# Kernel optimization log

Measured on AMD Instinct MI355X. Metric: run time of the kernel, lower is better.

The kernel has to match this reference:

```python
import jax, jax.numpy as jnp
from jax import lax
import numpy as np

EPS = 1e-5
RADIUS = 0.2
NPOINT = 1024
NSAMPLE = 32
B, N = 8, 8192


def furthest_point_sample(xyz, npoint):
    # xyz: (B,N,3) -> idx (B,npoint), start at index 0 (pytorch3d default)
    Bn, Nn, _ = xyz.shape
    def step(carry, _):
        dists, last = carry  # (B,N), (B,)
        lastpt = jnp.take_along_axis(xyz, last[:, None, None], axis=1)  # (B,1,3)
        d = jnp.sum((xyz - lastpt) ** 2, axis=-1)  # (B,N)
        dists = jnp.minimum(dists, d)
        nxt = jnp.argmax(dists, axis=-1).astype(jnp.int32)
        return (dists, nxt), last
    init = (jnp.full((Bn, Nn), jnp.inf, xyz.dtype), jnp.zeros((Bn,), jnp.int32))
    _, idxs = lax.scan(step, init, None, length=npoint)  # (npoint,B)
    return idxs.T  # (B,npoint)


def ball_query(radius, nsample, xyz, new_xyz):
    # first `nsample` points (by original index order) within radius; pad -> 0 (clamp of -1)
    Nn = xyz.shape[1]
    d2 = jnp.sum((new_xyz[:, :, None, :] - xyz[:, None, :, :]) ** 2, axis=-1)  # (B,S,N)
    valid = d2 < radius * radius
    score = jnp.where(valid, jnp.arange(Nn, dtype=jnp.int32), jnp.int32(Nn))  # smaller = earlier valid
    neg_vals, _ = lax.top_k(-score, nsample)  # picks nsample smallest scores
    idx = -neg_vals  # (B,S,nsample)
    idx = jnp.where(idx == Nn, 0, idx)  # pytorch3d pads with -1, then clamp(min=0) -> 0
    return idx


def bn_relu(x, g, be, m, v):
    # eval-mode BatchNorm over channel (last) dim + ReLU
    return jax.nn.relu((x - m) * (g / jnp.sqrt(v + EPS)) + be)


def setup_inputs() -> dict:
    key = jax.random.key(0)
    ks = jax.random.split(key, 4)
    xyz = jax.random.uniform(ks[0], (B, N, 3), dtype=jnp.float32)
    w1 = jax.random.normal(ks[1], (64, 3), dtype=jnp.float32) * 0.1
    w2 = jax.random.normal(ks[2], (64, 64), dtype=jnp.float32) * 0.1
    w3 = jax.random.normal(ks[3], (128, 64), dtype=jnp.float32) * 0.1
    z64, o64 = jnp.zeros((64,), jnp.float32), jnp.ones((64,), jnp.float32)
    z128, o128 = jnp.zeros((128,), jnp.float32), jnp.ones((128,), jnp.float32)
    return {
        "xyz": xyz,
        "w1": w1, "b1": z64, "g1": o64, "be1": z64, "m1": z64, "v1": o64,
        "w2": w2, "b2": z64, "g2": o64, "be2": z64, "m2": z64, "v2": o64,
        "w3": w3, "b3": z128, "g3": o128, "be3": z128, "m3": z128, "v3": o128,
    }


def reference(xyz, w1, b1, g1, be1, m1, v1, w2, b2, g2, be2, m2, v2, w3, b3, g3, be3, m3, v3):
    fps_idx = furthest_point_sample(xyz, NPOINT)  # (B,npoint)
    new_xyz = jnp.take_along_axis(xyz, fps_idx[:, :, None], axis=1)  # (B,npoint,3)
    idx = ball_query(RADIUS, NSAMPLE, xyz, new_xyz)  # (B,npoint,nsample)
    grouped_xyz = jax.vmap(lambda pts, i: pts[i])(xyz, idx)  # (B,npoint,nsample,3)
    # 1x1 conv MLP (channels-last) + eval BN + ReLU
    h = bn_relu(jnp.einsum('bsnc,oc->bsno', grouped_xyz, w1) + b1, g1, be1, m1, v1)
    h = bn_relu(jnp.einsum('bsnc,oc->bsno', h, w2) + b2, g2, be2, m2, v2)
    h = bn_relu(jnp.einsum('bsnc,oc->bsno', h, w3) + b3, g3, be3, m3, v3)
    new_features = jnp.max(h, axis=2)  # (B,npoint,128) max over nsample
    new_features = jnp.transpose(new_features, (0, 2, 1))  # (B,128,npoint) to match torch layout
    return new_xyz, new_features
```

## Files before the change

### kernel.cpp

```cpp
#include <hip/hip_runtime.h>

#define B 8
#define N 8192
#define S 1024
#define NS 32
#define THREADS 512
#define NCONS_BLK 248
#define NCONS_WAVE (NCONS_BLK * 8)
constexpr float BN_EPS = 1e-5f;

typedef float v2f __attribute__((ext_vector_type(2)));

struct KParams {
  const float* xyz;
  const float *w1, *b1, *g1, *be1, *m1, *v1;
  const float *w2, *b2, *g2, *be2, *m2, *v2;
  const float *w3, *b3, *g3, *be3, *m3, *v3;
  float* new_xyz;
  float* out_feat;
  float* ctrs;
  unsigned* prog;
};

__device__ __forceinline__ float wave_max_to_lane63(float x) {
  int v = __float_as_int(x);
#define DPP_MAX(ctrl)                                                     \
  v = __float_as_int(fmaxf(__int_as_float(v),                             \
      __int_as_float(__builtin_amdgcn_update_dpp(v, v, (ctrl), 0xf, 0xf, \
                                                 false))))
  DPP_MAX(0x111);
  DPP_MAX(0x112);
  DPP_MAX(0x114);
  DPP_MAX(0x118);
  DPP_MAX(0x142);
  DPP_MAX(0x143);
#undef DPP_MAX
  return __int_as_float(v);
}

__device__ __forceinline__ void producer(const KParams& P, char* smem, int b,
                                         int t, int lane, int w) {
#pragma clang fp contract(off)
  float4* s_xyz4 = (float4*)smem;
  float* s_ctr = (float*)(smem + 131072);
  unsigned long long(*s_red)[8] =
      (unsigned long long(*)[8])(smem + 131072 + 12288);
  const float* base = P.xyz + (size_t)b * N * 3;
  v2f X[8], Y[8], Z[8], D[8];
  const int p0 = t * 16;
  {
    const float4* src = (const float4*)(base + (size_t)p0 * 3);
    float buf[48];
#pragma unroll
    for (int i = 0; i < 12; ++i) {
      float4 v = src[i];
      buf[4 * i + 0] = v.x; buf[4 * i + 1] = v.y;
      buf[4 * i + 2] = v.z; buf[4 * i + 3] = v.w;
    }
#pragma unroll
    for (int k = 0; k < 16; ++k)
      s_xyz4[p0 + k] =
          make_float4(buf[3 * k], buf[3 * k + 1], buf[3 * k + 2], 0.f);
#pragma unroll
    for (int i = 0; i < 8; ++i) {
      X[i] = (v2f){buf[6 * i + 0], buf[6 * i + 3]};
      Y[i] = (v2f){buf[6 * i + 1], buf[6 * i + 4]};
      Z[i] = (v2f){buf[6 * i + 2], buf[6 * i + 5]};
      D[i] = (v2f){3.4e38f, 3.4e38f};
    }
  }
  float lx = base[0], ly = base[1], lz = base[2];
  if (t == 0) { s_ctr[0] = lx; s_ctr[1] = ly; s_ctr[2] = lz; }
  for (int r = 1; r < S; ++r) {
    v2f lx2 = lx, ly2 = ly, lz2 = lz;
#pragma unroll
    for (int i = 0; i < 8; ++i) {
      v2f dx = X[i] - lx2, dy = Y[i] - ly2, dz = Z[i] - lz2;
      v2f d = (dx * dx + dy * dy) + dz * dz;
      D[i] = __builtin_elementwise_min(D[i], d);
    }
    float n1[8], n2[4], n3[2];
#pragma unroll
    for (int i = 0; i < 8; ++i) n1[i] = fmaxf(D[i].x, D[i].y);
#pragma unroll
    for (int i = 0; i < 4; ++i) n2[i] = fmaxf(n1[2 * i], n1[2 * i + 1]);
    n3[0] = fmaxf(n2[0], n2[1]);
    n3[1] = fmaxf(n2[2], n2[3]);
    float m = fmaxf(n3[0], n3[1]);
    int c3 = (n3[0] < m) ? 1 : 0;
    float n2s = c3 ? n2[2] : n2[0];
    int c2 = (n2s < m) ? 1 : 0;
    float n1a = c3 ? n1[4] : n1[0];
    float n1b = c3 ? n1[6] : n1[2];
    float n1s = c2 ? n1b : n1a;
    int c1 = (n1s < m) ? 1 : 0;
    float dx0 = c3 ? D[4].x : D[0].x;
    float dx1 = c3 ? D[5].x : D[1].x;
    float dx2 = c3 ? D[6].x : D[2].x;
    float dx3 = c3 ? D[7].x : D[3].x;
    float dxa = c2 ? dx2 : dx0;
    float dxb = c2 ? dx3 : dx1;
    float dxs = c1 ? dxb : dxa;
    int c0 = (dxs < m) ? 1 : 0;
    int li = 8 * c3 + 4 * c2 + 2 * c1 + c0;
    float wm = wave_max_to_lane63(m);
    float wavemax =
        __int_as_float(__builtin_amdgcn_readlane(__float_as_int(wm), 63));
    unsigned long long bal = __ballot(m == wavemax);
    int firstlane = (int)__builtin_ctzll(bal);
    int widx = __builtin_amdgcn_readlane(p0 + li, firstlane);
    unsigned long long key =
        ((unsigned long long)__float_as_uint(wavemax) << 32) |
        (unsigned)(8191 - widx);
    if (lane == 0) s_red[r & 1][w] = key;
    __syncthreads();
    {
      const unsigned long long* sr = s_red[r & 1];
      unsigned long long k0 = sr[0], k1 = sr[1], k2 = sr[2], k3 = sr[3];
      unsigned long long k4 = sr[4], k5 = sr[5], k6 = sr[6], k7 = sr[7];
      unsigned long long a = k0 > k1 ? k0 : k1;
      unsigned long long c = k2 > k3 ? k2 : k3;
      unsigned long long e = k4 > k5 ? k4 : k5;
      unsigned long long g = k6 > k7 ? k6 : k7;
      unsigned long long ac = a > c ? a : c;
      unsigned long long eg = e > g ? e : g;
      unsigned long long kmax = ac > eg ? ac : eg;
      const int bi = 8191 - (int)(unsigned)(kmax & 0xffffffffull);
      float4 cc = s_xyz4[bi];
      lx = cc.x; ly = cc.y; lz = cc.z;
    }
    if (t == 0) {
      s_ctr[r * 3 + 0] = lx; s_ctr[r * 3 + 1] = ly; s_ctr[r * 3 + 2] = lz;
    }
    if (w == 0 && (r & 7) == 7) {
      int cbase = (r - 7) * 3;
      if (lane < 24) {
        float v = s_ctr[cbase + lane];
        __hip_atomic_store(P.ctrs + (size_t)b * (S * 3) + cbase + lane, v,
                           __ATOMIC_RELAXED, __HIP_MEMORY_SCOPE_AGENT);
      }
      if (lane == 0)
        __hip_atomic_store(&P.prog[b * 64], (unsigned)(r + 1),
                           __ATOMIC_RELEASE, __HIP_MEMORY_SCOPE_AGENT);
    }
  }
  __syncthreads();
  float* o = P.new_xyz + (size_t)b * S * 3;
  for (int i = t; i < (S * 3) / 4; i += THREADS)
    ((float4*)o)[i] = ((const float4*)s_ctr)[i];
}

__device__ __forceinline__ void consumer(const KParams& P, char* smem, int cid,
                                         int t, int lane, int w) {
#pragma clang fp contract(off)
  constexpr float R2 = (float)(0.2 * 0.2);
  float* h = (float*)smem + w * (NS * 64);
  float* cs = (float*)smem + 8 * NS * 64 + w * (NS * 4);
  const unsigned gw = cid * 8 + w;
  float sv1 = P.g1[lane] / sqrtf(P.v1[lane] + BN_EPS);
  float bb1 = (P.b1[lane] - P.m1[lane]) * sv1 + P.be1[lane];
  float w1x = P.w1[lane * 3 + 0] * sv1, w1y = P.w1[lane * 3 + 1] * sv1,
        w1z = P.w1[lane * 3 + 2] * sv1;
  float sv2 = P.g2[lane] / sqrtf(P.v2[lane] + BN_EPS);
  float bb2 = (P.b2[lane] - P.m2[lane]) * sv2 + P.be2[lane];
  float W2[64];
#pragma unroll
  for (int k = 0; k < 64; k += 4) {
    float4 q = *(const float4*)(P.w2 + lane * 64 + k);
    W2[k + 0] = q.x * sv2; W2[k + 1] = q.y * sv2;
    W2[k + 2] = q.z * sv2; W2[k + 3] = q.w * sv2;
  }
  float sva = P.g3[lane] / sqrtf(P.v3[lane] + BN_EPS);
  float bba = (P.b3[lane] - P.m3[lane]) * sva + P.be3[lane];
  float svb = P.g3[lane + 64] / sqrtf(P.v3[lane + 64] + BN_EPS);
  float bbb = (P.b3[lane + 64] - P.m3[lane + 64]) * svb + P.be3[lane + 64];
  float Wa[64], Wb[64];
#pragma unroll
  for (int k = 0; k < 64; k += 4) {
    float4 qa = *(const float4*)(P.w3 + lane * 64 + k);
    Wa[k + 0] = qa.x * sva; Wa[k + 1] = qa.y * sva;
    Wa[k + 2] = qa.z * sva; Wa[k + 3] = qa.w * sva;
    float4 qb = *(const float4*)(P.w3 + (lane + 64) * 64 + k);
    Wb[k + 0] = qb.x * svb; Wb[k + 1] = qb.y * svb;
    Wb[k + 2] = qb.z * svb; Wb[k + 3] = qb.w * svb;
  }
  for (unsigned c = gw; c < B * S; c += NCONS_WAVE) {
    const int b = c & 7;
    const int s = c >> 3;
    while (__hip_atomic_load(&P.prog[b * 64], __ATOMIC_RELAXED,
                             __HIP_MEMORY_SCOPE_AGENT) <= (unsigned)s)
      __builtin_amdgcn_s_sleep(2);
    (void)__hip_atomic_load(&P.prog[b * 64], __ATOMIC_ACQUIRE,
                            __HIP_MEMORY_SCOPE_AGENT);
    const float* cg = P.ctrs + (size_t)b * (S * 3) + s * 3;
    float cx = __hip_atomic_load(cg + 0, __ATOMIC_RELAXED,
                                 __HIP_MEMORY_SCOPE_AGENT);
    float cy = __hip_atomic_load(cg + 1, __ATOMIC_RELAXED,
                                 __HIP_MEMORY_SCOPE_AGENT);
    float cz = __hip_atomic_load(cg + 2, __ATOMIC_RELAXED,
                                 __HIP_MEMORY_SCOPE_AGENT);
    const float* base = P.xyz + (size_t)b * N * 3;
    int cnt = 0;
    for (int c0 = 0; c0 < N && cnt < NS; c0 += 64) {
      int p = c0 + lane;
      float x = base[p * 3], y = base[p * 3 + 1], z = base[p * 3 + 2];
      float dx = x - cx, dy = y - cy, dz = z - cz;
      float d = (dx * dx + dy * dy) + dz * dz;
      bool v = d < R2;
      unsigned long long mk = __ballot(v);
      int rank = cnt + __popcll(mk & ((1ull << lane) - 1ull));
      if (v && rank < NS) {
        cs[rank * 4 + 0] = x; cs[rank * 4 + 1] = y; cs[rank * 4 + 2] = z;
      }
      cnt += (int)__popcll(mk);
    }
    if (cnt < NS) {
      float x0 = base[0], y0 = base[1], z0 = base[2];
      for (int j = cnt + lane; j < NS; j += 64) {
        cs[j * 4 + 0] = x0; cs[j * 4 + 1] = y0; cs[j * 4 + 2] = z0;
      }
    }
    for (int n = 0; n < NS; ++n) {
      float a = fmaf(w1x, cs[n * 4 + 0],
                     fmaf(w1y, cs[n * 4 + 1], fmaf(w1z, cs[n * 4 + 2], bb1)));
      h[n * 64 + lane] = fmaxf(a, 0.f);
    }
    for (int n = 0; n < NS; ++n) {
      float acc = bb2;
#pragma unroll
      for (int k = 0; k < 64; k += 4) {
        float4 q = *(const float4*)(h + n * 64 + k);
        acc = fmaf(W2[k + 0], q.x, acc);
        acc = fmaf(W2[k + 1], q.y, acc);
        acc = fmaf(W2[k + 2], q.z, acc);
        acc = fmaf(W2[k + 3], q.w, acc);
      }
      h[n * 64 + lane] = fmaxf(acc, 0.f);
    }
    float mxa = 0.f, mxb = 0.f;
    for (int n = 0; n < NS; ++n) {
      float acca = bba, accb = bbb;
#pragma unroll
      for (int k = 0; k < 64; k += 4) {
        float4 q = *(const float4*)(h + n * 64 + k);
        acca = fmaf(Wa[k + 0], q.x, acca);
        acca = fmaf(Wa[k + 1], q.y, acca);
        acca = fmaf(Wa[k + 2], q.z, acca);
        acca = fmaf(Wa[k + 3], q.w, acca);
        accb = fmaf(Wb[k + 0], q.x, accb);
        accb = fmaf(Wb[k + 1], q.y, accb);
        accb = fmaf(Wb[k + 2], q.z, accb);
        accb = fmaf(Wb[k + 3], q.w, accb);
      }
      mxa = fmaxf(mxa, acca);
      mxb = fmaxf(mxb, accb);
    }
    P.out_feat[((size_t)b * 128 + lane) * S + s] = mxa;
    P.out_feat[((size_t)b * 128 + 64 + lane) * S + s] = mxb;
  }
}

__global__ void __attribute__((amdgpu_flat_work_group_size(THREADS, THREADS),
                               amdgpu_waves_per_eu(2, 2)))
k_fused(KParams P) {
  extern __shared__ char smem[];
  const int t = threadIdx.x;
  const int lane = t & 63;
  const int w = t >> 6;
  if (blockIdx.x < B)
    producer(P, smem, blockIdx.x, t, lane, w);
  else
    consumer(P, smem, blockIdx.x - B, t, lane, w);
}

extern "C" void kernel_launch(void* const* d_in, const int* in_sizes, int n_in,
                              void* d_out, int out_size, void* d_ws,
                              size_t ws_size, hipStream_t stream) {
  KParams P;
  P.xyz = (const float*)d_in[0];
  P.w1 = (const float*)d_in[1];  P.b1 = (const float*)d_in[2];
  P.g1 = (const float*)d_in[3];  P.be1 = (const float*)d_in[4];
  P.m1 = (const float*)d_in[5];  P.v1 = (const float*)d_in[6];
  P.w2 = (const float*)d_in[7];  P.b2 = (const float*)d_in[8];
  P.g2 = (const float*)d_in[9];  P.be2 = (const float*)d_in[10];
  P.m2 = (const float*)d_in[11]; P.v2 = (const float*)d_in[12];
  P.w3 = (const float*)d_in[13]; P.b3 = (const float*)d_in[14];
  P.g3 = (const float*)d_in[15]; P.be3 = (const float*)d_in[16];
  P.m3 = (const float*)d_in[17]; P.v3 = (const float*)d_in[18];
  float* out = (float*)d_out;
  P.new_xyz = out;
  P.out_feat = out + (size_t)B * S * 3;
  P.prog = (unsigned*)d_ws;
  P.ctrs = (float*)((char*)d_ws + 2048);

  hipMemsetAsync(d_ws, 0, 2048, stream);

  void* args[] = {&P};
  dim3 grid(B + NCONS_BLK), blk(THREADS);
  size_t shmem = 131072 + 12288 + 256;
  hipError_t e = hipLaunchCooperativeKernel((const void*)k_fused, grid, blk,
                                            args, (unsigned)shmem, stream);
  if (e != hipSuccess) {
    k_fused<<<grid, blk, shmem, stream>>>(P);
  }
}
```

Measured before the change: 1.049 ms.

## Halve block size so FPS threads own more points, with lagged progress publish

Block size drops from 512 to 256 threads. Each FPS producer thread now holds 32 points in registers, and the cross-wave argmax reduces over 4 waves instead of 8. This is meant to shorten the per-iteration barrier and reduction on the serial FPS critical path, at the cost of more per-thread arithmetic and register pressure, and half as many consumer waves per block. The progress counter is now published one batch late, ahead of the newest center stores, with a final publish after the loop. Consumer spin-wait sleep is also lengthened to reduce polling traffic.

```diff
diff --git a/kernel.cpp b/kernel.cpp
--- a/kernel.cpp
+++ b/kernel.cpp
@@ -4,9 +4,9 @@
 #define N 8192
 #define S 1024
 #define NS 32
-#define THREADS 512
+#define THREADS 256
 #define NCONS_BLK 248
-#define NCONS_WAVE (NCONS_BLK * 8)
+#define NCONS_WAVE (NCONS_BLK * 4)
 constexpr float BN_EPS = 1e-5f;
 
 typedef float v2f __attribute__((ext_vector_type(2)));
@@ -43,26 +43,26 @@
 #pragma clang fp contract(off)
   float4* s_xyz4 = (float4*)smem;
   float* s_ctr = (float*)(smem + 131072);
-  unsigned long long(*s_red)[8] =
-      (unsigned long long(*)[8])(smem + 131072 + 12288);
+  unsigned long long(*s_red)[4] =
+      (unsigned long long(*)[4])(smem + 131072 + 12288);
   const float* base = P.xyz + (size_t)b * N * 3;
-  v2f X[8], Y[8], Z[8], D[8];
-  const int p0 = t * 16;
+  v2f X[16], Y[16], Z[16], D[16];
+  const int p0 = t * 32;
   {
     const float4* src = (const float4*)(base + (size_t)p0 * 3);
-    float buf[48];
-#pragma unroll
-    for (int i = 0; i < 12; ++i) {
+    float buf[96];
+#pragma unroll
+    for (int i = 0; i < 24; ++i) {
       float4 v = src[i];
       buf[4 * i + 0] = v.x; buf[4 * i + 1] = v.y;
       buf[4 * i + 2] = v.z; buf[4 * i + 3] = v.w;
     }
 #pragma unroll
-    for (int k = 0; k < 16; ++k)
+    for (int k = 0; k < 32; ++k)
       s_xyz4[p0 + k] =
           make_float4(buf[3 * k], buf[3 * k + 1], buf[3 * k + 2], 0.f);
 #pragma unroll
-    for (int i = 0; i < 8; ++i) {
+    for (int i = 0; i < 16; ++i) {
       X[i] = (v2f){buf[6 * i + 0], buf[6 * i + 3]};
       Y[i] = (v2f){buf[6 * i + 1], buf[6 * i + 4]};
       Z[i] = (v2f){buf[6 * i + 2], buf[6 * i + 5]};
@@ -74,35 +74,53 @@
   for (int r = 1; r < S; ++r) {
     v2f lx2 = lx, ly2 = ly, lz2 = lz;
 #pragma unroll
-    for (int i = 0; i < 8; ++i) {
+    for (int i = 0; i < 16; ++i) {
       v2f dx = X[i] - lx2, dy = Y[i] - ly2, dz = Z[i] - lz2;
       v2f d = (dx * dx + dy * dy) + dz * dz;
       D[i] = __builtin_elementwise_min(D[i], d);
     }
-    float n1[8], n2[4], n3[2];
-#pragma unroll
-    for (int i = 0; i < 8; ++i) n1[i] = fmaxf(D[i].x, D[i].y);
-#pragma unroll
-    for (int i = 0; i < 4; ++i) n2[i] = fmaxf(n1[2 * i], n1[2 * i + 1]);
-    n3[0] = fmaxf(n2[0], n2[1]);
-    n3[1] = fmaxf(n2[2], n2[3]);
-    float m = fmaxf(n3[0], n3[1]);
-    int c3 = (n3[0] < m) ? 1 : 0;
-    float n2s = c3 ? n2[2] : n2[0];
+    float n1[16], n2[8], n3[4], n4[2];
+#pragma unroll
+    for (int i = 0; i < 16; ++i) n1[i] = fmaxf(D[i].x, D[i].y);
+#pragma unroll
+    for (int i = 0; i < 8; ++i) n2[i] = fmaxf(n1[2 * i], n1[2 * i + 1]);
+#pragma unroll
+    for (int i = 0; i < 4; ++i) n3[i] = fmaxf(n2[2 * i], n2[2 * i + 1]);
+    n4[0] = fmaxf(n3[0], n3[1]);
+    n4[1] = fmaxf(n3[2], n3[3]);
+    float m = fmaxf(n4[0], n4[1]);
+    int c4 = (n4[0] < m) ? 1 : 0;
+    float n3s = c4 ? n3[2] : n3[0];
+    int c3 = (n3s < m) ? 1 : 0;
+    float n2a = c4 ? n2[4] : n2[0];
+    float n2b = c4 ? n2[6] : n2[2];
+    float n2s = c3 ? n2b : n2a;
     int c2 = (n2s < m) ? 1 : 0;
-    float n1a = c3 ? n1[4] : n1[0];
-    float n1b = c3 ? n1[6] : n1[2];
-    float n1s = c2 ? n1b : n1a;
+    float n1a = c4 ? n1[8] : n1[0];
+    float n1b = c4 ? n1[10] : n1[2];
+    float n1c = c4 ? n1[12] : n1[4];
+    float n1d = c4 ? n1[14] : n1[6];
+    float n1e = c3 ? n1c : n1a;
+    float n1f = c3 ? n1d : n1b;
+    float n1s = c2 ? n1f : n1e;
     int c1 = (n1s < m) ? 1 : 0;
-    float dx0 = c3 ? D[4].x : D[0].x;
-    float dx1 = c3 ? D[5].x : D[1].x;
-    float dx2 = c3 ? D[6].x : D[2].x;
-    float dx3 = c3 ? D[7].x : D[3].x;
-    float dxa = c2 ? dx2 : dx0;
-    float dxb = c2 ? dx3 : dx1;
-    float dxs = c1 ? dxb : dxa;
+    float e0 = c4 ? D[8].x : D[0].x;
+    float e1 = c4 ? D[9].x : D[1].x;
+    float e2 = c4 ? D[10].x : D[2].x;
+    float e3 = c4 ? D[11].x : D[3].x;
+    float e4 = c4 ? D[12].x : D[4].x;
+    float e5 = c4 ? D[13].x : D[5].x;
+    float e6 = c4 ? D[14].x : D[6].x;
+    float e7 = c4 ? D[15].x : D[7].x;
+    float f0 = c3 ? e4 : e0;
+    float f1 = c3 ? e5 : e1;
+    float f2 = c3 ? e6 : e2;
+    float f3 = c3 ? e7 : e3;
+    float g0 = c2 ? f2 : f0;
+    float g1 = c2 ? f3 : f1;
+    float dxs = c1 ? g1 : g0;
     int c0 = (dxs < m) ? 1 : 0;
-    int li = 8 * c3 + 4 * c2 + 2 * c1 + c0;
+    int li = 16 * c4 + 8 * c3 + 4 * c2 + 2 * c1 + c0;
     float wm = wave_max_to_lane63(m);
     float wavemax =
         __int_as_float(__builtin_amdgcn_readlane(__float_as_int(wm), 63));
@@ -117,14 +135,9 @@
     {
       const unsigned long long* sr = s_red[r & 1];
       unsigned long long k0 = sr[0], k1 = sr[1], k2 = sr[2], k3 = sr[3];
-      unsigned long long k4 = sr[4], k5 = sr[5], k6 = sr[6], k7 = sr[7];
       unsigned long long a = k0 > k1 ? k0 : k1;
       unsigned long long c = k2 > k3 ? k2 : k3;
-      unsigned long long e = k4 > k5 ? k4 : k5;
-      unsigned long long g = k6 > k7 ? k6 : k7;
-      unsigned long long ac = a > c ? a : c;
-      unsigned long long eg = e > g ? e : g;
-      unsigned long long kmax = ac > eg ? ac : eg;
+      unsigned long long kmax = a > c ? a : c;
       const int bi = 8191 - (int)(unsigned)(kmax & 0xffffffffull);
       float4 cc = s_xyz4[bi];
       lx = cc.x; ly = cc.y; lz = cc.z;
@@ -133,18 +146,21 @@
       s_ctr[r * 3 + 0] = lx; s_ctr[r * 3 + 1] = ly; s_ctr[r * 3 + 2] = lz;
     }
     if (w == 0 && (r & 7) == 7) {
+      int k8 = r >> 3;
+      if (lane == 0 && k8 >= 1)
+        __hip_atomic_store(&P.prog[b * 64], (unsigned)(k8 * 8),
+                           __ATOMIC_RELEASE, __HIP_MEMORY_SCOPE_AGENT);
       int cbase = (r - 7) * 3;
-      if (lane < 24) {
-        float v = s_ctr[cbase + lane];
-        __hip_atomic_store(P.ctrs + (size_t)b * (S * 3) + cbase + lane, v,
-                           __ATOMIC_RELAXED, __HIP_MEMORY_SCOPE_AGENT);
-      }
-      if (lane == 0)
-        __hip_atomic_store(&P.prog[b * 64], (unsigned)(r + 1),
-                           __ATOMIC_RELEASE, __HIP_MEMORY_SCOPE_AGENT);
+      if (lane < 24)
+        __hip_atomic_store(P.ctrs + (size_t)b * (S * 3) + cbase + lane,
+                           s_ctr[cbase + lane], __ATOMIC_RELAXED,
+                           __HIP_MEMORY_SCOPE_AGENT);
     }
   }
   __syncthreads();
+  if (w == 0 && lane == 0)
+    __hip_atomic_store(&P.prog[b * 64], (unsigned)S, __ATOMIC_RELEASE,
+                       __HIP_MEMORY_SCOPE_AGENT);
   float* o = P.new_xyz + (size_t)b * S * 3;
   for (int i = t; i < (S * 3) / 4; i += THREADS)
     ((float4*)o)[i] = ((const float4*)s_ctr)[i];
@@ -155,8 +171,8 @@
 #pragma clang fp contract(off)
   constexpr float R2 = (float)(0.2 * 0.2);
   float* h = (float*)smem + w * (NS * 64);
-  float* cs = (float*)smem + 8 * NS * 64 + w * (NS * 4);
-  const unsigned gw = cid * 8 + w;
+  float* cs = (float*)smem + 4 * NS * 64 + w * (NS * 4);
+  const unsigned gw = cid * 4 + w;
   float sv1 = P.g1[lane] / sqrtf(P.v1[lane] + BN_EPS);
   float bb1 = (P.b1[lane] - P.m1[lane]) * sv1 + P.be1[lane];
   float w1x = P.w1[lane * 3 + 0] * sv1, w1y = P.w1[lane * 3 + 1] * sv1,
@@ -189,7 +205,7 @@
     const int s = c >> 3;
     while (__hip_atomic_load(&P.prog[b * 64], __ATOMIC_RELAXED,
                              __HIP_MEMORY_SCOPE_AGENT) <= (unsigned)s)
-      __builtin_amdgcn_s_sleep(2);
+      __builtin_amdgcn_s_sleep(8);
     (void)__hip_atomic_load(&P.prog[b * 64], __ATOMIC_ACQUIRE,
                             __HIP_MEMORY_SCOPE_AGENT);
     const float* cg = P.ctrs + (size_t)b * (S * 3) + s * 3;
```

After: 950.4 us. -9.4%, faster.
